# Kernel tuning notes

Measured on AMD Instinct MI355X. Metric: run time of the kernel, lower is better.

Reference implementation:

```python
import jax, jax.numpy as jnp
import numpy as np

T, B, E, H, V = 50, 64, 1024, 1024, 32000
NL = 2


def setup_inputs() -> dict:
    key = jax.random.key(0)
    ks = jax.random.split(key, 16)
    def rn(k, shape, fan_in):
        return jax.random.normal(k, shape, jnp.float32) * (1.0 / np.sqrt(fan_in))
    return {
        "word": jax.random.randint(ks[0], (B,), 0, V),
        "seq": jax.random.randint(ks[1], (T, B), 0, V),
        "emb": jax.random.normal(ks[2], (V, E), jnp.float32) * 0.05,
        "w2h_W": rn(ks[3], (H, E), E),
        "w2h_b": jnp.zeros((H,), jnp.float32),
        "W_ih0": rn(ks[4], (4 * H, 2 * E), 2 * E),
        "W_hh0": rn(ks[5], (4 * H, H), H),
        "b_ih0": jnp.zeros((4 * H,), jnp.float32),
        "b_hh0": jnp.zeros((4 * H,), jnp.float32),
        "W_ih1": rn(ks[6], (4 * H, H), H),
        "W_hh1": rn(ks[7], (4 * H, H), H),
        "b_ih1": jnp.zeros((4 * H,), jnp.float32),
        "b_hh1": jnp.zeros((4 * H,), jnp.float32),
        "dec_W": rn(ks[8], (V, H), H),
        "dec_b": jnp.zeros((V,), jnp.float32),
    }


def _lstm_layer(x, Wih, Whh, bih, bhh, h0, c0):
    """x: [T,B,D] -> hs: [T,B,H]. PyTorch gate order: i,f,g,o."""
    b = bih + bhh
    # precompute input contribution for all timesteps (one big GEMM)
    xg = jnp.einsum('tbd,gd->tbg', x, Wih) + b  # [T,B,4H]

    def step(carry, xt):
        h, c = carry
        gates = xt + h @ Whh.T
        i, f, g, o = jnp.split(gates, 4, axis=-1)
        c = jax.nn.sigmoid(f) * c + jax.nn.sigmoid(i) * jnp.tanh(g)
        h = jax.nn.sigmoid(o) * jnp.tanh(c)
        return (h, c), h

    (hT, cT), hs = jax.lax.scan(step, (h0, c0), xg)
    return hs, hT, cT


def reference(word, seq, emb, w2h_W, w2h_b, W_ih0, W_hh0, b_ih0, b_hh0,
              W_ih1, W_hh1, b_ih1, b_hh1, dec_W, dec_b):
    word_emb = emb[word]            # [B,E]
    seq_emb = emb[seq]              # [T,B,E]
    # init_hidden: c = word2hidden(word_emb) expanded over layers, h = zeros
    c0 = word_emb @ w2h_W.T + w2h_b          # [B,H]
    h0 = jnp.zeros_like(c0)
    # use_input: concat word_emb to every timestep input
    x0 = jnp.concatenate(
        [jnp.broadcast_to(word_emb[None], (T, B, E)), seq_emb], axis=-1)  # [T,B,2E]
    hs0, h0T, c0T = _lstm_layer(x0, W_ih0, W_hh0, b_ih0, b_hh0, h0, c0)
    hs1, h1T, c1T = _lstm_layer(hs0, W_ih1, W_hh1, b_ih1, b_hh1, h0, c0)
    outputs = hs1.reshape(T * B, H)
    decoded = outputs @ dec_W.T + dec_b      # [T*B, V]
    h_final = jnp.stack([h0T, h1T], 0)       # [NL,B,H]
    c_final = jnp.stack([c0T, c1T], 0)
    return decoded, h_final, c_final
```

## Files before the change

kernel.cpp:

```cpp
#include <hip/hip_runtime.h>
#include <cstddef>


static constexpr int T_ = 50, B_ = 64, E_ = 1024, H_ = 1024, V_ = 32000;
static constexpr int G_ = 4096;

typedef unsigned short u16;
typedef unsigned int u32;
typedef unsigned long long u64;
typedef __attribute__((ext_vector_type(8))) short bf16x8;
typedef __attribute__((ext_vector_type(8))) unsigned short u16x8;
typedef __attribute__((ext_vector_type(4))) float f32x4;

__device__ __forceinline__ int perm_g(int n) {
  return ((n >> 4) & 3) * H_ + (n >> 6) * 16 + (n & 15);
}
__device__ __forceinline__ u16 bf16_rn(float x) {
  union { float f; unsigned u; } a; a.f = x;
  unsigned r = a.u + 0x7fffu + ((a.u >> 16) & 1u);
  return (u16)(r >> 16);
}
__device__ __forceinline__ float bf16_f(u16 h) {
  union { float f; unsigned u; } a; a.u = ((unsigned)h) << 16;
  return a.f;
}
__device__ __forceinline__ float sigm(float x) { return 1.f / (1.f + __expf(-x)); }

__global__ void fill_zero(float* p, int n) {
  int i = blockIdx.x * blockDim.x + threadIdx.x;
  if (i < n) p[i] = 0.f;
}
__global__ void bias_perm(const float* a, const float* b, float* dst) {
  int n = blockIdx.x * 256 + threadIdx.x;
  int s = perm_g(n);
  dst[n] = a[s] + b[s];
}

__global__ void conv_w(const float* __restrict__ src, int srcld, int coloff,
                       const int* __restrict__ gidx, int PERM, int rows,
                       u16* __restrict__ dst) {
  int idx = blockIdx.x * 256 + threadIdx.x;
  int r = idx >> 7, kc = (idx & 127) << 3;
  if (r >= rows) return;
  int s = gidx ? gidx[r] : (PERM ? perm_g(r) : r);
  const float* p = src + (size_t)s * srcld + coloff + kc;
  float4 v0 = *(const float4*)p, v1 = *(const float4*)(p + 4);
  float vv[8] = {v0.x, v0.y, v0.z, v0.w, v1.x, v1.y, v1.z, v1.w};
  u16 hi[8], lo[8];
#pragma unroll
  for (int i = 0; i < 8; ++i) {
    hi[i] = bf16_rn(vv[i]);
    lo[i] = bf16_rn(vv[i] - bf16_f(hi[i]));
  }
  u16x8 c0, c1;
#pragma unroll
  for (int i = 0; i < 4; ++i) {
    c0[2 * i] = hi[i];     c0[2 * i + 1] = lo[i];
    c1[2 * i] = hi[4 + i]; c1[2 * i + 1] = lo[4 + i];
  }
  int seg = kc >> 5;
  int ch0 = (kc >> 2) & 7;
  size_t base = (size_t)r * 2048 + seg * 64;
  *(u16x8*)&dst[base + (size_t)((ch0 ^ (r & 7)) << 3)] = c0;
  *(u16x8*)&dst[base + (size_t)(((ch0 | 1) ^ (r & 7)) << 3)] = c1;
}

template<int BM, int BN, int BK, int TM, int TN>
__launch_bounds__(256)
__global__ void gemm_nt(
    const float* __restrict__ A, const int* __restrict__ Aidx, int lda,
    const float* __restrict__ W, int ldw, int koff,
    const float* __restrict__ bias, float* __restrict__ C, int ldc,
    int M, int N, int K) {
  constexpr int TX = BN / TN;
  constexpr int TY = BM / TM;
  static_assert(TX * TY == 256, "thread geometry");
  __shared__ float As[BK][BM + 4];
  __shared__ float Ws[BK][BN + 4];
  const int tid = threadIdx.x;
  const int tx = tid % TX, ty = tid / TX;
  const int m0 = blockIdx.y * BM, n0 = blockIdx.x * BN;
  float acc[TM][TN];
#pragma unroll
  for (int i = 0; i < TM; ++i)
#pragma unroll
    for (int j = 0; j < TN; ++j) acc[i][j] = 0.f;
  constexpr int AV = (BM * BK) / 4;
  constexpr int WV = (BN * BK) / 4;
  constexpr int KV = BK / 4;
  for (int k0 = 0; k0 < K; k0 += BK) {
#pragma unroll
    for (int lp = 0; lp < (AV + 255) / 256; ++lp) {
      int e = tid + lp * 256;
      if (e < AV) {
        int r = e / KV, kq = e % KV;
        int m = m0 + r;
        float4 v = make_float4(0.f, 0.f, 0.f, 0.f);
        if (m < M) {
          int row = Aidx ? Aidx[m] : m;
          v = *(const float4*)&A[(size_t)row * lda + k0 + kq * 4];
        }
        As[kq * 4 + 0][r] = v.x; As[kq * 4 + 1][r] = v.y;
        As[kq * 4 + 2][r] = v.z; As[kq * 4 + 3][r] = v.w;
      }
    }
#pragma unroll
    for (int lp = 0; lp < (WV + 255) / 256; ++lp) {
      int e = tid + lp * 256;
      if (e < WV) {
        int cc = e / KV, kq = e % KV;
        int n = n0 + cc;
        float4 v = make_float4(0.f, 0.f, 0.f, 0.f);
        if (n < N)
          v = *(const float4*)&W[(size_t)n * ldw + koff + k0 + kq * 4];
        Ws[kq * 4 + 0][cc] = v.x; Ws[kq * 4 + 1][cc] = v.y;
        Ws[kq * 4 + 2][cc] = v.z; Ws[kq * 4 + 3][cc] = v.w;
      }
    }
    __syncthreads();
#pragma unroll
    for (int kk = 0; kk < BK; ++kk) {
      float a[TM], b[TN];
#pragma unroll
      for (int i = 0; i < TM; ++i) a[i] = As[kk][ty * TM + i];
#pragma unroll
      for (int j = 0; j < TN; ++j) b[j] = Ws[kk][tx * TN + j];
#pragma unroll
      for (int i = 0; i < TM; ++i)
#pragma unroll
        for (int j = 0; j < TN; ++j)
          acc[i][j] += a[i] * b[j];
    }
    __syncthreads();
  }
#pragma unroll
  for (int i = 0; i < TM; ++i) {
    int m = m0 + ty * TM + i;
    if (m >= M) continue;
#pragma unroll
    for (int j = 0; j < TN; ++j) {
      int n = n0 + tx * TN + j;
      if (n >= N) continue;
      float v = acc[i][j];
      if (bias) v += bias[n];
      C[(size_t)m * ldc + n] = v;
    }
  }
}

__launch_bounds__(256)
__global__ void gemm_bt(const u16* __restrict__ A, int Mrows,
                        const u16* __restrict__ Wb,
                        const float* __restrict__ bias,
                        const float* __restrict__ Dadd, int ldd, int dmask,
                        float* __restrict__ C, int ldc, int N, int nbx,
                        int mt, int ord) {
  __shared__ u16 lsA[128 * 64];
  __shared__ u16 lsB[128 * 64];

  int nwg = gridDim.x, bid = blockIdx.x;
  int q = nwg >> 3, r = nwg & 7;
  int xcd = bid & 7, base = bid >> 3;
  int wg = (xcd < r ? xcd * (q + 1) : r * (q + 1) + (xcd - r) * q) + base;
  int bx, by;
  if (ord) { by = wg % mt; bx = wg / mt; } else { bx = wg % nbx; by = wg / nbx; }
  const int m0 = by * 128, n0 = bx * 128;

  const int tid = threadIdx.x, w = tid >> 6, l = tid & 63;
  const int lr = l & 15, lq = l >> 4;
  const int wm = (w >> 1) * 64, wn = (w & 1) * 64;

  f32x4 acc[4][4] = {};

  for (int kt = 0; kt < 32; ++kt) {
#pragma unroll
    for (int i = 0; i < 4; ++i) {
      int rb = w * 32 + i * 8;
      int gm = m0 + rb + (l >> 3);
      if (gm > Mrows - 1) gm = Mrows - 1;
      const u16* ga = A + (size_t)gm * 2048 + kt * 64 + (l & 7) * 8;
      __builtin_amdgcn_global_load_lds(
          (const __attribute__((address_space(1))) void*)ga,
          (__attribute__((address_space(3))) void*)(lsA + rb * 64), 16, 0, 0);
      const u16* gb = Wb + (size_t)(n0 + rb + (l >> 3)) * 2048 + kt * 64 + (l & 7) * 8;
      __builtin_amdgcn_global_load_lds(
          (const __attribute__((address_space(1))) void*)gb,
          (__attribute__((address_space(3))) void*)(lsB + rb * 64), 16, 0, 0);
    }
    asm volatile("s_waitcnt vmcnt(0)" ::: "memory");
    __syncthreads();

    bf16x8 af[4][2], bfr[4][2];
#pragma unroll
    for (int i = 0; i < 4; ++i) {
      int ar = wm + i * 16 + lr;
#pragma unroll
      for (int s = 0; s < 2; ++s)
        af[i][s] = *(const bf16x8*)&lsA[ar * 64 + (((s << 2) + lq) ^ (ar & 7)) * 8];
    }
#pragma unroll
    for (int j = 0; j < 4; ++j) {
      int br = wn + j * 16 + lr;
#pragma unroll
      for (int s = 0; s < 2; ++s)
        bfr[j][s] = *(const bf16x8*)&lsB[br * 64 + (((s << 2) + lq) ^ (br & 7)) * 8];
    }
#pragma unroll
    for (int i = 0; i < 4; ++i)
#pragma unroll
      for (int j = 0; j < 4; ++j) {
        acc[i][j] = __builtin_amdgcn_mfma_f32_16x16x32_bf16(af[i][0], bfr[j][0], acc[i][j], 0, 0, 0);
        acc[i][j] = __builtin_amdgcn_mfma_f32_16x16x32_bf16(af[i][1], bfr[j][1], acc[i][j], 0, 0, 0);
      }
    __syncthreads();
  }

#pragma unroll
  for (int i = 0; i < 4; ++i) {
    int mbase = m0 + wm + i * 16 + lq * 4;
#pragma unroll
    for (int j = 0; j < 4; ++j) {
      int n = n0 + wn + j * 16 + lr;
      float badd = bias ? bias[n] : 0.f;
#pragma unroll
      for (int rr = 0; rr < 4; ++rr) {
        int m = mbase + rr;
        if (m >= Mrows) continue;
        float v = acc[i][j][rr] + badd;
        if (Dadd) {
          int dr = (dmask < 0) ? m : (m & dmask);
          v += Dadd[(size_t)dr * ldd + n];
        }
        C[(size_t)m * ldc + n] = v;
      }
    }
  }
}

__launch_bounds__(256)
__global__ void gemm_sp(
    const float* __restrict__ A, int lda,
    const float* __restrict__ W, int ldw,
    const float* __restrict__ bias,
    float* __restrict__ C, int ldc, int M, int N, int K, int nbx) {
  __shared__ u16 As_h[128][40], As_l[128][40];
  __shared__ u16 Ws_h[128][40], Ws_l[128][40];
  int nwg = gridDim.x, bid = blockIdx.x;
  int q = nwg >> 3, r = nwg & 7;
  int xcd = bid & 7, base = bid >> 3;
  int wg = (xcd < r ? xcd * (q + 1) : r * (q + 1) + (xcd - r) * q) + base;
  int bx = wg % nbx, by = wg / nbx;
  const int m0 = by * 128, n0 = bx * 128;
  const int tid = threadIdx.x;
  const int wave = tid >> 6, lane = tid & 63;
  const int lr = lane & 15, lq = lane >> 4;
  const int wm = (wave >> 1) * 64, wn = (wave & 1) * 64;
  f32x4 acc[4][4] = {};
  for (int k0 = 0; k0 < K; k0 += 32) {
#pragma unroll
    for (int lp = 0; lp < 4; ++lp) {
      int s = tid + lp * 256;
      int row = s >> 3, kq = s & 7;
      float4 v = make_float4(0.f, 0.f, 0.f, 0.f);
      int gm = m0 + row;
      if (gm < M)
        v = *(const float4*)&A[(size_t)gm * lda + k0 + kq * 4];
      u16 h0 = bf16_rn(v.x), h1 = bf16_rn(v.y), h2 = bf16_rn(v.z), h3 = bf16_rn(v.w);
      u16 l0 = bf16_rn(v.x - bf16_f(h0)), l1 = bf16_rn(v.y - bf16_f(h1));
      u16 l2 = bf16_rn(v.z - bf16_f(h2)), l3 = bf16_rn(v.w - bf16_f(h3));
      *(uint2*)&As_h[row][kq * 4] =
          make_uint2((u32)h0 | ((u32)h1 << 16), (u32)h2 | ((u32)h3 << 16));
      *(uint2*)&As_l[row][kq * 4] =
          make_uint2((u32)l0 | ((u32)l1 << 16), (u32)l2 | ((u32)l3 << 16));
    }
#pragma unroll
    for (int lp = 0; lp < 4; ++lp) {
      int s = tid + lp * 256;
      int col = s >> 3, kq = s & 7;
      int n = n0 + col;
      float4 v = make_float4(0.f, 0.f, 0.f, 0.f);
      if (n < N)
        v = *(const float4*)&W[(size_t)n * ldw + k0 + kq * 4];
      u16 h0 = bf16_rn(v.x), h1 = bf16_rn(v.y), h2 = bf16_rn(v.z), h3 = bf16_rn(v.w);
      u16 l0 = bf16_rn(v.x - bf16_f(h0)), l1 = bf16_rn(v.y - bf16_f(h1));
      u16 l2 = bf16_rn(v.z - bf16_f(h2)), l3 = bf16_rn(v.w - bf16_f(h3));
      *(uint2*)&Ws_h[col][kq * 4] =
          make_uint2((u32)h0 | ((u32)h1 << 16), (u32)h2 | ((u32)h3 << 16));
      *(uint2*)&Ws_l[col][kq * 4] =
          make_uint2((u32)l0 | ((u32)l1 << 16), (u32)l2 | ((u32)l3 << 16));
    }
    __syncthreads();
    bf16x8 ah[4], al[4], bh[4], bl[4];
#pragma unroll
    for (int i = 0; i < 4; ++i) {
      ah[i] = *(const bf16x8*)&As_h[wm + i * 16 + lr][lq * 8];
      al[i] = *(const bf16x8*)&As_l[wm + i * 16 + lr][lq * 8];
    }
#pragma unroll
    for (int j = 0; j < 4; ++j) {
      bh[j] = *(const bf16x8*)&Ws_h[wn + j * 16 + lr][lq * 8];
      bl[j] = *(const bf16x8*)&Ws_l[wn + j * 16 + lr][lq * 8];
    }
#pragma unroll
    for (int i = 0; i < 4; ++i)
#pragma unroll
      for (int j = 0; j < 4; ++j) {
        acc[i][j] = __builtin_amdgcn_mfma_f32_16x16x32_bf16(ah[i], bh[j], acc[i][j], 0, 0, 0);
        acc[i][j] = __builtin_amdgcn_mfma_f32_16x16x32_bf16(ah[i], bl[j], acc[i][j], 0, 0, 0);
        acc[i][j] = __builtin_amdgcn_mfma_f32_16x16x32_bf16(al[i], bh[j], acc[i][j], 0, 0, 0);
      }
    __syncthreads();
  }
#pragma unroll
  for (int i = 0; i < 4; ++i) {
    int mbase = m0 + wm + i * 16 + lq * 4;
#pragma unroll
    for (int j = 0; j < 4; ++j) {
      int n = n0 + wn + j * 16 + lr;
      if (n >= N) continue;
      float badd = bias ? bias[n] : 0.f;
#pragma unroll
      for (int rr = 0; rr < 4; ++rr) {
        int m = mbase + rr;
        if (m >= M) continue;
        C[(size_t)m * ldc + n] = acc[i][j][rr] + badd;
      }
    }
  }
}

template<bool EMIT>
__launch_bounds__(512, 1)
__global__ void rnn_reg2(const u16* __restrict__ Wb, const float* __restrict__ xgall,
                         float* __restrict__ cL, float* __restrict__ hL,
                         u32* __restrict__ hs, float* __restrict__ hsf,
                         u32* __restrict__ flags, int T) {
  __shared__ float partial[8][32][68];

  const int bid = blockIdx.x;
  const int x = bid & 7, ii = bid >> 3;
  const int ct = x * 8 + (ii & 7);
  const int rg = ii >> 3;
  const int tid = threadIdx.x, w = tid >> 6, l = tid & 63;
  const int lr = l & 15, lq = l >> 4;

  const u16* WbB = Wb + (size_t)(ct * 64) * 2048;
  bf16x8 bfrag[8][4];
#pragma unroll
  for (int s = 0; s < 8; ++s)
#pragma unroll
    for (int nt = 0; nt < 4; ++nt) {
      int row = nt * 16 + lr;
      int seg = w * 4 + (s >> 1);
      int cis = ((((s & 1) << 2) + lq) ^ (lr & 7));
      bfrag[s][nt] = *(const bf16x8*)&WbB[(size_t)row * 2048 + seg * 64 + cis * 8];
    }

  const int cm = tid >> 4, cu = tid & 15;
  const int m_c = rg * 32 + cm;
  const int unit = ct * 16 + cu;
  float creg = cL[m_c * H_ + unit];

  for (int t = 0; t < T; ++t) {
    const float* xg = xgall + (size_t)t * ((size_t)B_ * G_);
    float xgv[4];
#pragma unroll
    for (int g = 0; g < 4; ++g)
      xgv[g] = xg[(size_t)m_c * G_ + ct * 64 + g * 16 + cu];

    if (t) {
      if (w == 0) {
        const u32 tgt = (u32)t;
        int guard = 0;
        for (;;) {
          u32 v = __hip_atomic_load(flags + (size_t)((rg << 6) + l) * 32,
                                    __ATOMIC_RELAXED, __HIP_MEMORY_SCOPE_AGENT);
          if (__all(v >= tgt)) break;
          if (++guard > (1 << 24)) break;
          __builtin_amdgcn_s_sleep(2);
        }
      }
    }
    __syncthreads();

    const u32* hp = hs + (size_t)t * (B_ * 1024);

    f32x4 acc[2][4] = {};
    {
      bf16x8 af[4][2];
#pragma unroll
      for (int s = 0; s < 4; ++s)
#pragma unroll
        for (int mt = 0; mt < 2; ++mt) {
          int m = rg * 32 + mt * 16 + lr;
          int seg = w * 4 + (s >> 1);
          int cis = ((((s & 1) << 2) + lq) ^ (lr & 7));
          const u64* pq = (const u64*)(hp + (size_t)m * 1024 + seg * 32 + cis * 4);
          u64 q0 = __hip_atomic_load(pq, __ATOMIC_RELAXED, __HIP_MEMORY_SCOPE_AGENT);
          u64 q1 = __hip_atomic_load(pq + 1, __ATOMIC_RELAXED, __HIP_MEMORY_SCOPE_AGENT);
          union { u64 q[2]; bf16x8 v; } cvt;
          cvt.q[0] = q0; cvt.q[1] = q1;
          af[s][mt] = cvt.v;
        }
#pragma unroll
      for (int s = 0; s < 4; ++s)
#pragma unroll
        for (int mt = 0; mt < 2; ++mt)
#pragma unroll
          for (int nt = 0; nt < 4; ++nt)
            acc[mt][nt] = __builtin_amdgcn_mfma_f32_16x16x32_bf16(
                af[s][mt], bfrag[s][nt], acc[mt][nt], 0, 0, 0);
    }
    {
      bf16x8 af[4][2];
#pragma unroll
      for (int s = 0; s < 4; ++s)
#pragma unroll
        for (int mt = 0; mt < 2; ++mt) {
          int m = rg * 32 + mt * 16 + lr;
          int seg = w * 4 + ((s + 4) >> 1);
          int cis = ((((s & 1) << 2) + lq) ^ (lr & 7));
          const u64* pq = (const u64*)(hp + (size_t)m * 1024 + seg * 32 + cis * 4);
          u64 q0 = __hip_atomic_load(pq, __ATOMIC_RELAXED, __HIP_MEMORY_SCOPE_AGENT);
          u64 q1 = __hip_atomic_load(pq + 1, __ATOMIC_RELAXED, __HIP_MEMORY_SCOPE_AGENT);
          union { u64 q[2]; bf16x8 v; } cvt;
          cvt.q[0] = q0; cvt.q[1] = q1;
          af[s][mt] = cvt.v;
        }
#pragma unroll
      for (int s = 0; s < 4; ++s)
#pragma unroll
        for (int mt = 0; mt < 2; ++mt)
#pragma unroll
          for (int nt = 0; nt < 4; ++nt)
            acc[mt][nt] = __builtin_amdgcn_mfma_f32_16x16x32_bf16(
                af[s][mt], bfrag[s + 4][nt], acc[mt][nt], 0, 0, 0);
    }

#pragma unroll
    for (int mt = 0; mt < 2; ++mt)
#pragma unroll
      for (int nt = 0; nt < 4; ++nt)
#pragma unroll
        for (int rr = 0; rr < 4; ++rr)
          partial[w][mt * 16 + lq * 4 + rr][nt * 16 + lr] = acc[mt][nt][rr];
    __syncthreads();

    float g4[4];
#pragma unroll
    for (int g = 0; g < 4; ++g) {
      float ssum = xgv[g];
#pragma unroll
      for (int p = 0; p < 8; ++p) ssum += partial[p][cm][g * 16 + cu];
      g4[g] = ssum;
    }
    float cn = sigm(g4[1]) * creg + sigm(g4[0]) * tanhf(g4[2]);
    float hn = sigm(g4[3]) * tanhf(cn);
    creg = cn;
    if (EMIT) hsf[(size_t)t * (B_ * H_) + m_c * H_ + unit] = hn;
    if (t == T - 1) { cL[m_c * H_ + unit] = cn; hL[m_c * H_ + unit] = hn; }
    u16 hh = bf16_rn(hn);
    u16 hl2 = bf16_rn(hn - bf16_f(hh));
    u32 packed = (u32)hh | ((u32)hl2 << 16);
    u32* hnext = hs + (size_t)(t + 1) * (B_ * 1024);
    u32 hidx = m_c * 1024 + ((unit >> 5) << 5) +
               ((((unit >> 2) & 7) ^ (m_c & 7)) << 2) + (unit & 3);
    __hip_atomic_store(hnext + hidx, packed, __ATOMIC_RELAXED, __HIP_MEMORY_SCOPE_AGENT);

    if (t < T - 1) {
      asm volatile("s_waitcnt vmcnt(0)" ::: "memory");
      __syncthreads();
      if (tid == 0)
        __hip_atomic_store(flags + (size_t)((rg << 6) + ct) * 32, (u32)(t + 1),
                           __ATOMIC_RELAXED, __HIP_MEMORY_SCOPE_AGENT);
    }
  }
}

__launch_bounds__(256)
__global__ void rnn_step(const u16* __restrict__ hprev, const u16* __restrict__ Wb,
                         const float* __restrict__ xg,
                         float* __restrict__ c, float* __restrict__ hf,
                         u32* __restrict__ hout) {
  __shared__ char smem[32768];
  u16* lsA = (u16*)smem;
  u16* lsB = (u16*)(smem + 16384);
  const int nt = blockIdx.x, n0 = nt * 64;
  const int tid = threadIdx.x, w = tid >> 6, l = tid & 63;
  const int lr = l & 15, lq = l >> 4;
  f32x4 acc[4] = {};
  for (int kt = 0; kt < 16; ++kt) {
#pragma unroll
    for (int i = 0; i < 4; ++i) {
      int rb = w * 16 + i * 4;
      const u16* ga = hprev + (size_t)(rb + (l >> 4)) * 2048 + kt * 128 + (l & 15) * 8;
      __builtin_amdgcn_global_load_lds(
          (const __attribute__((address_space(1))) void*)ga,
          (__attribute__((address_space(3))) void*)(lsA + rb * 128), 16, 0, 0);
      const u16* gb = Wb + (size_t)(n0 + rb + (l >> 4)) * 2048 + kt * 128 + (l & 15) * 8;
      __builtin_amdgcn_global_load_lds(
          (const __attribute__((address_space(1))) void*)gb,
          (__attribute__((address_space(3))) void*)(lsB + rb * 128), 16, 0, 0);
    }
    asm volatile("s_waitcnt vmcnt(0)" ::: "memory");
    __syncthreads();
    bf16x8 af[4];
    int ar = w * 16 + lr;
#pragma unroll
    for (int s = 0; s < 4; ++s)
      af[s] = *(const bf16x8*)&lsA[ar * 128 + (s >> 1) * 64 + ((((s & 1) << 2) + lq) ^ (ar & 7)) * 8];
#pragma unroll
    for (int j = 0; j < 4; ++j) {
      int br = j * 16 + lr;
#pragma unroll
      for (int s = 0; s < 4; ++s) {
        bf16x8 bv = *(const bf16x8*)&lsB[br * 128 + (s >> 1) * 64 + ((((s & 1) << 2) + lq) ^ (br & 7)) * 8];
        acc[j] = __builtin_amdgcn_mfma_f32_16x16x32_bf16(af[s], bv, acc[j], 0, 0, 0);
      }
    }
    __syncthreads();
  }
  float* gsh = (float*)smem;
#pragma unroll
  for (int j = 0; j < 4; ++j)
#pragma unroll
    for (int rr = 0; rr < 4; ++rr)
      gsh[(w * 16 + lq * 4 + rr) * 68 + j * 16 + lr] = acc[j][rr];
  __syncthreads();
  const int ui = tid & 15, mq = tid >> 4;
#pragma unroll
  for (int mr = 0; mr < 4; ++mr) {
    int m = mr * 16 + mq;
    float gi = gsh[m * 68 + 0 + ui]  + xg[(size_t)m * G_ + n0 + 0 + ui];
    float gf = gsh[m * 68 + 16 + ui] + xg[(size_t)m * G_ + n0 + 16 + ui];
    float gg = gsh[m * 68 + 32 + ui] + xg[(size_t)m * G_ + n0 + 32 + ui];
    float go = gsh[m * 68 + 48 + ui] + xg[(size_t)m * G_ + n0 + 48 + ui];
    int unit = nt * 16 + ui;
    int ci = m * H_ + unit;
    float cn = sigm(gf) * c[ci] + sigm(gi) * tanhf(gg);
    float hn = sigm(go) * tanhf(cn);
    c[ci] = cn;
    hf[ci] = hn;
    u16 hh = bf16_rn(hn);
    u16 hl = bf16_rn(hn - bf16_f(hh));
    u32 hidx = m * 1024 + ((unit >> 5) << 5) +
               ((((unit >> 2) & 7) ^ (m & 7)) << 2) + (unit & 3);
    hout[hidx] = (u32)hh | ((u32)hl << 16);
  }
}

extern "C" void kernel_launch(void* const* d_in, const int* in_sizes, int n_in,
                              void* d_out, int out_size, void* d_ws, size_t ws_size,
                              hipStream_t stream) {
  const int*   word  = (const int*)  d_in[0];
  const int*   seq   = (const int*)  d_in[1];
  const float* emb   = (const float*)d_in[2];
  const float* w2h_W = (const float*)d_in[3];
  const float* w2h_b = (const float*)d_in[4];
  const float* W_ih0 = (const float*)d_in[5];
  const float* W_hh0 = (const float*)d_in[6];
  const float* b_ih0 = (const float*)d_in[7];
  const float* b_hh0 = (const float*)d_in[8];
  const float* W_ih1 = (const float*)d_in[9];
  const float* W_hh1 = (const float*)d_in[10];
  const float* b_ih1 = (const float*)d_in[11];
  const float* b_hh1 = (const float*)d_in[12];
  const float* dec_W = (const float*)d_in[13];
  const float* dec_b = (const float*)d_in[14];

  float* out = (float*)d_out;
  float* hL0 = out + 102400000;
  float* hL1 = hL0 + B_ * H_;
  float* cL0 = out + 102531072;
  float* cL1 = cL0 + B_ * H_;

  float* xg0      = out;
  u16*   x0w_bf   = (u16*)(out + 13200000);
  u16*   x0seq_bf = (u16*)(out + 13300000);
  u32*   hs0slots = (u32*)(out + 16600000);
  u16*   wih0a_bf = (u16*)(out + 20000000);
  u16*   wih0b_bf = (u16*)(out + 24200000);
  u16*   wih1_bf  = (u16*)(out + 28400000);
  u16*   whh0_bf  = (u16*)(out + 32600000);
  u16*   whh1_bf  = (u16*)(out + 36800000);
  float* y_w      = out + 73800000;
  float* bias0p   = out + 74400000;
  float* bias1p   = out + 74410000;
  float* xg1      = out + 87560192;
  u32*   flg0     = (u32*)(out + 101000000);
  u32*   flg1     = (u32*)(out + 101004096);
  u32*   hbfA     = (u32*)(out + 101100000);
  u32*   hbfB     = (u32*)(out + 101200000);

  const size_t need_hs1  = (size_t)T_ * B_ * H_ * 4;
  const size_t need_full = (size_t)V_ * 2048 * 2 + (size_t)(T_ + 1) * B_ * 1024 * 4;
  const bool tier1 = ws_size >= need_full;
  const bool tier2 = !tier1 && ws_size >= need_hs1;

  u16*   decW_bf  = (u16*)d_ws;
  u32*   hs1slots = (u32*)d_ws + (size_t)V_ * 1024;
  float* hs1f     = (float*)d_ws;

  fill_zero<<<32, 256, 0, stream>>>(out + 101000000, 8192);
  fill_zero<<<256, 256, 0, stream>>>((float*)hs0slots, 65536);
  if (tier1) fill_zero<<<256, 256, 0, stream>>>((float*)hs1slots, 65536);
  bias_perm<<<16, 256, 0, stream>>>(b_ih0, b_hh0, bias0p);
  bias_perm<<<16, 256, 0, stream>>>(b_ih1, b_hh1, bias1p);

  gemm_nt<64, 64, 16, 4, 4><<<dim3(16, 1), 256, 0, stream>>>(
      emb, word, E_, w2h_W, E_, 0, w2h_b, cL0, H_, B_, H_, E_);
  gemm_nt<64, 64, 16, 4, 4><<<dim3(16, 1), 256, 0, stream>>>(
      emb, word, E_, w2h_W, E_, 0, w2h_b, cL1, H_, B_, H_, E_);

  conv_w<<<2048, 256, 0, stream>>>(W_ih0, 2 * E_, 0,  nullptr, 1, G_, wih0a_bf);
  conv_w<<<2048, 256, 0, stream>>>(W_ih0, 2 * E_, E_, nullptr, 1, G_, wih0b_bf);
  conv_w<<<2048, 256, 0, stream>>>(W_ih1, H_, 0, nullptr, 1, G_, wih1_bf);
  conv_w<<<2048, 256, 0, stream>>>(W_hh0, H_, 0, nullptr, 1, G_, whh0_bf);
  conv_w<<<2048, 256, 0, stream>>>(W_hh1, H_, 0, nullptr, 1, G_, whh1_bf);
  conv_w<<<32,   256, 0, stream>>>(emb, E_, 0, word, 0, B_, x0w_bf);
  conv_w<<<1600, 256, 0, stream>>>(emb, E_, 0, seq, 0, T_ * B_, x0seq_bf);
  if (tier1)
    conv_w<<<16000, 256, 0, stream>>>(dec_W, H_, 0, nullptr, 0, V_, decW_bf);

  gemm_bt<<<32, 256, 0, stream>>>(x0w_bf, B_, wih0a_bf, bias0p,
                                  nullptr, 0, -1, y_w, G_, G_, 32, 1, 0);
  gemm_bt<<<800, 256, 0, stream>>>(x0seq_bf, T_ * B_, wih0b_bf, nullptr,
                                   y_w, G_, 63, xg0, G_, G_, 32, 25, 0);

  rnn_reg2<false><<<128, 512, 0, stream>>>(
      whh0_bf, xg0, cL0, hL0, hs0slots, nullptr, flg0, T_);

  gemm_bt<<<800, 256, 0, stream>>>((const u16*)(hs0slots + (size_t)B_ * 1024),
                                   T_ * B_, wih1_bf, bias1p,
                                   nullptr, 0, -1, xg1, G_, G_, 32, 25, 0);

  if (tier1) {
    rnn_reg2<false><<<128, 512, 0, stream>>>(
        whh1_bf, xg1, cL1, hL1, hs1slots, nullptr, flg1, T_);
    gemm_bt<<<6250, 256, 0, stream>>>((const u16*)(hs1slots + (size_t)B_ * 1024),
                                      T_ * B_, decW_bf, dec_b,
                                      nullptr, 0, -1, out, V_, V_, 250, 25, 1);
  } else if (tier2) {
    rnn_reg2<true><<<128, 512, 0, stream>>>(
        whh1_bf, xg1, cL1, hL1, hs0slots, hs1f, flg1, T_);
    gemm_sp<<<6250, 256, 0, stream>>>(
        hs1f, H_, dec_W, H_, dec_b, out, V_, T_ * B_, V_, H_, 250);
  } else {
    for (int t = 0; t < T_; ++t) {
      const u16* hp = t ? (const u16*)((t & 1) ? hbfA : hbfB) : (const u16*)hs0slots;
      u32* ho = (t & 1) ? hbfB : hbfA;
      rnn_step<<<64, 256, 0, stream>>>(
          hp, whh1_bf, xg1 + (size_t)t * B_ * G_, cL1, hL1, ho);
      gemm_sp<<<250, 256, 0, stream>>>(
          hL1, H_, dec_W, H_, dec_b, out + (size_t)t * B_ * V_, V_, B_, V_, H_, 250);
    }
  }
}
```

Before: 1.837 ms.

## Fuse both LSTM layers into one persistent wavefront-pipelined recurrent kernel

Runs layer 0 and layer 1 recurrences concurrently in one persistent launch of 256 blocks: layer-1 blocks wait on layer-0 flags for step t+1 and compute the input projection W_ih1·h0 inline with register-resident weights, instead of waiting for layer 0 to finish and running a separate xg1 GEMM. This overlaps the two sequential recurrences and removes the intermediate GEMM and its xg1 traffic. The costs are doubled register pressure for layer-1 blocks holding two weight fragment sets, twice the MFMA work per step for those blocks, and reliance on all 256 blocks being co-resident for the spin-wait to avoid deadlock.

```diff
diff --git a/kernel.cpp b/kernel.cpp
--- a/kernel.cpp
+++ b/kernel.cpp
@@ -329,23 +329,60 @@
   }
 }
 
-template<bool EMIT>
+__device__ __forceinline__ void gemm_half(
+    const u32* __restrict__ hp, int rg, int w, int lr, int lq,
+    const bf16x8 (&bfr)[8][4], f32x4 (&acc)[2][4]) {
+#pragma unroll
+  for (int half = 0; half < 2; ++half) {
+    bf16x8 af[4][2];
+#pragma unroll
+    for (int s = 0; s < 4; ++s)
+#pragma unroll
+      for (int mt = 0; mt < 2; ++mt) {
+        int m = rg * 32 + mt * 16 + lr;
+        int seg = w * 4 + ((s + half * 4) >> 1);
+        int cis = ((((s & 1) << 2) + lq) ^ (lr & 7));
+        const u64* pq = (const u64*)(hp + (size_t)m * 1024 + seg * 32 + cis * 4);
+        u64 q0 = __hip_atomic_load(pq, __ATOMIC_RELAXED, __HIP_MEMORY_SCOPE_AGENT);
+        u64 q1 = __hip_atomic_load(pq + 1, __ATOMIC_RELAXED, __HIP_MEMORY_SCOPE_AGENT);
+        union { u64 q[2]; bf16x8 v; } cvt;
+        cvt.q[0] = q0; cvt.q[1] = q1;
+        af[s][mt] = cvt.v;
+      }
+#pragma unroll
+    for (int s = 0; s < 4; ++s)
+#pragma unroll
+      for (int mt = 0; mt < 2; ++mt)
+#pragma unroll
+        for (int nt = 0; nt < 4; ++nt)
+          acc[mt][nt] = __builtin_amdgcn_mfma_f32_16x16x32_bf16(
+              af[s][mt], bfr[s + half * 4][nt], acc[mt][nt], 0, 0, 0);
+  }
+}
+
+template<bool DUAL, bool EMIT>
 __launch_bounds__(512, 1)
-__global__ void rnn_reg2(const u16* __restrict__ Wb, const float* __restrict__ xgall,
-                         float* __restrict__ cL, float* __restrict__ hL,
-                         u32* __restrict__ hs, float* __restrict__ hsf,
-                         u32* __restrict__ flags, int T) {
+__global__ void rnn_dual(const u16* __restrict__ Whh0b, const u16* __restrict__ Whh1b,
+                         const u16* __restrict__ Wih1b,
+                         const float* __restrict__ xg0all, const float* __restrict__ bias1p,
+                         float* __restrict__ cL0, float* __restrict__ hL0,
+                         float* __restrict__ cL1, float* __restrict__ hL1,
+                         u32* __restrict__ h0s, u32* __restrict__ h1s,
+                         float* __restrict__ hsf,
+                         u32* __restrict__ flg0, u32* __restrict__ flg1, int T) {
   __shared__ float partial[8][32][68];
 
   const int bid = blockIdx.x;
-  const int x = bid & 7, ii = bid >> 3;
-  const int ct = x * 8 + (ii & 7);
-  const int rg = ii >> 3;
+  const int x = bid & 7, j = bid >> 3;
+  const int layer = DUAL ? (j & 1) : 0;
+  const int idx = DUAL ? (j >> 1) : j;
+  const int ct = x * 8 + (idx & 7);
+  const int rg = idx >> 3;
   const int tid = threadIdx.x, w = tid >> 6, l = tid & 63;
   const int lr = l & 15, lq = l >> 4;
 
-  const u16* WbB = Wb + (size_t)(ct * 64) * 2048;
-  bf16x8 bfrag[8][4];
+  const u16* WbA = (layer ? Whh1b : Whh0b) + (size_t)(ct * 64) * 2048;
+  bf16x8 bfragA[8][4];
 #pragma unroll
   for (int s = 0; s < 8; ++s)
 #pragma unroll
@@ -353,88 +390,91 @@
       int row = nt * 16 + lr;
       int seg = w * 4 + (s >> 1);
       int cis = ((((s & 1) << 2) + lq) ^ (lr & 7));
-      bfrag[s][nt] = *(const bf16x8*)&WbB[(size_t)row * 2048 + seg * 64 + cis * 8];
-    }
+      bfragA[s][nt] = *(const bf16x8*)&WbA[(size_t)row * 2048 + seg * 64 + cis * 8];
+    }
+  bf16x8 bfragX[8][4];
+  if (DUAL && layer) {
+    const u16* WbX = Wih1b + (size_t)(ct * 64) * 2048;
+#pragma unroll
+    for (int s = 0; s < 8; ++s)
+#pragma unroll
+      for (int nt = 0; nt < 4; ++nt) {
+        int row = nt * 16 + lr;
+        int seg = w * 4 + (s >> 1);
+        int cis = ((((s & 1) << 2) + lq) ^ (lr & 7));
+        bfragX[s][nt] = *(const bf16x8*)&WbX[(size_t)row * 2048 + seg * 64 + cis * 8];
+      }
+  }
 
   const int cm = tid >> 4, cu = tid & 15;
   const int m_c = rg * 32 + cm;
   const int unit = ct * 16 + cu;
+  float* cL = layer ? cL1 : cL0;
+  float* hL = layer ? hL1 : hL0;
+  u32* hsl = layer ? h1s : h0s;
+  u32* flgS = layer ? flg1 : flg0;
   float creg = cL[m_c * H_ + unit];
+  float bset[4];
+  if (layer) {
+#pragma unroll
+    for (int g = 0; g < 4; ++g)
+      bset[g] = bias1p[ct * 64 + g * 16 + cu];
+  }
 
   for (int t = 0; t < T; ++t) {
-    const float* xg = xgall + (size_t)t * ((size_t)B_ * G_);
     float xgv[4];
-#pragma unroll
-    for (int g = 0; g < 4; ++g)
-      xgv[g] = xg[(size_t)m_c * G_ + ct * 64 + g * 16 + cu];
-
-    if (t) {
-      if (w == 0) {
+    if (!layer) {
+      const float* xg = xg0all + (size_t)t * ((size_t)B_ * G_);
+#pragma unroll
+      for (int g = 0; g < 4; ++g)
+        xgv[g] = xg[(size_t)m_c * G_ + ct * 64 + g * 16 + cu];
+    } else {
+#pragma unroll
+      for (int g = 0; g < 4; ++g) xgv[g] = bset[g];
+    }
+
+    if (w == 0) {
+      if (layer) {
+        const u32 tgt0 = (u32)(t + 1);
+        int guard = 0;
+        for (;;) {
+          u32 v = __hip_atomic_load(flg0 + (size_t)((rg << 6) + l) * 32,
+                                    __ATOMIC_RELAXED, __HIP_MEMORY_SCOPE_AGENT);
+          if (__all(v >= tgt0)) break;
+          if (++guard > (1 << 23)) break;
+          __builtin_amdgcn_s_sleep(2);
+        }
+        if (t) {
+          const u32 tgt1 = (u32)t;
+          guard = 0;
+          for (;;) {
+            u32 v = __hip_atomic_load(flg1 + (size_t)((rg << 6) + l) * 32,
+                                      __ATOMIC_RELAXED, __HIP_MEMORY_SCOPE_AGENT);
+            if (__all(v >= tgt1)) break;
+            if (++guard > (1 << 23)) break;
+            __builtin_amdgcn_s_sleep(2);
+          }
+        }
+      } else if (t) {
         const u32 tgt = (u32)t;
         int guard = 0;
         for (;;) {
-          u32 v = __hip_atomic_load(flags + (size_t)((rg << 6) + l) * 32,
+          u32 v = __hip_atomic_load(flg0 + (size_t)((rg << 6) + l) * 32,
                                     __ATOMIC_RELAXED, __HIP_MEMORY_SCOPE_AGENT);
           if (__all(v >= tgt)) break;
-          if (++guard > (1 << 24)) break;
+          if (++guard > (1 << 23)) break;
           __builtin_amdgcn_s_sleep(2);
         }
       }
     }
     __syncthreads();
 
-    const u32* hp = hs + (size_t)t * (B_ * 1024);
-
     f32x4 acc[2][4] = {};
-    {
-      bf16x8 af[4][2];
-#pragma unroll
-      for (int s = 0; s < 4; ++s)
-#pragma unroll
-        for (int mt = 0; mt < 2; ++mt) {
-          int m = rg * 32 + mt * 16 + lr;
-          int seg = w * 4 + (s >> 1);
-          int cis = ((((s & 1) << 2) + lq) ^ (lr & 7));
-          const u64* pq = (const u64*)(hp + (size_t)m * 1024 + seg * 32 + cis * 4);
-          u64 q0 = __hip_atomic_load(pq, __ATOMIC_RELAXED, __HIP_MEMORY_SCOPE_AGENT);
-          u64 q1 = __hip_atomic_load(pq + 1, __ATOMIC_RELAXED, __HIP_MEMORY_SCOPE_AGENT);
-          union { u64 q[2]; bf16x8 v; } cvt;
-          cvt.q[0] = q0; cvt.q[1] = q1;
-          af[s][mt] = cvt.v;
-        }
-#pragma unroll
-      for (int s = 0; s < 4; ++s)
-#pragma unroll
-        for (int mt = 0; mt < 2; ++mt)
-#pragma unroll
-          for (int nt = 0; nt < 4; ++nt)
-            acc[mt][nt] = __builtin_amdgcn_mfma_f32_16x16x32_bf16(
-                af[s][mt], bfrag[s][nt], acc[mt][nt], 0, 0, 0);
-    }
-    {
-      bf16x8 af[4][2];
-#pragma unroll
-      for (int s = 0; s < 4; ++s)
-#pragma unroll
-        for (int mt = 0; mt < 2; ++mt) {
-          int m = rg * 32 + mt * 16 + lr;
-          int seg = w * 4 + ((s + 4) >> 1);
-          int cis = ((((s & 1) << 2) + lq) ^ (lr & 7));
-          const u64* pq = (const u64*)(hp + (size_t)m * 1024 + seg * 32 + cis * 4);
-          u64 q0 = __hip_atomic_load(pq, __ATOMIC_RELAXED, __HIP_MEMORY_SCOPE_AGENT);
-          u64 q1 = __hip_atomic_load(pq + 1, __ATOMIC_RELAXED, __HIP_MEMORY_SCOPE_AGENT);
-          union { u64 q[2]; bf16x8 v; } cvt;
-          cvt.q[0] = q0; cvt.q[1] = q1;
-          af[s][mt] = cvt.v;
-        }
-#pragma unroll
-      for (int s = 0; s < 4; ++s)
-#pragma unroll
-        for (int mt = 0; mt < 2; ++mt)
-#pragma unroll
-          for (int nt = 0; nt < 4; ++nt)
-            acc[mt][nt] = __builtin_amdgcn_mfma_f32_16x16x32_bf16(
-                af[s][mt], bfrag[s + 4][nt], acc[mt][nt], 0, 0, 0);
+    if (layer) {
+      gemm_half(h1s + (size_t)t * (B_ * 1024), rg, w, lr, lq, bfragA, acc);
+      gemm_half(h0s + (size_t)(t + 1) * (B_ * 1024), rg, w, lr, lq, bfragX, acc);
+    } else {
+      gemm_half(h0s + (size_t)t * (B_ * 1024), rg, w, lr, lq, bfragA, acc);
     }
 
 #pragma unroll
@@ -457,21 +497,21 @@
     float cn = sigm(g4[1]) * creg + sigm(g4[0]) * tanhf(g4[2]);
     float hn = sigm(g4[3]) * tanhf(cn);
     creg = cn;
-    if (EMIT) hsf[(size_t)t * (B_ * H_) + m_c * H_ + unit] = hn;
+    if (EMIT && layer) hsf[(size_t)t * (B_ * H_) + m_c * H_ + unit] = hn;
     if (t == T - 1) { cL[m_c * H_ + unit] = cn; hL[m_c * H_ + unit] = hn; }
     u16 hh = bf16_rn(hn);
     u16 hl2 = bf16_rn(hn - bf16_f(hh));
     u32 packed = (u32)hh | ((u32)hl2 << 16);
-    u32* hnext = hs + (size_t)(t + 1) * (B_ * 1024);
+    u32* hnext = hsl + (size_t)(t + 1) * (B_ * 1024);
     u32 hidx = m_c * 1024 + ((unit >> 5) << 5) +
                ((((unit >> 2) & 7) ^ (m_c & 7)) << 2) + (unit & 3);
     __hip_atomic_store(hnext + hidx, packed, __ATOMIC_RELAXED, __HIP_MEMORY_SCOPE_AGENT);
 
-    if (t < T - 1) {
+    if (!layer || t < T - 1) {
       asm volatile("s_waitcnt vmcnt(0)" ::: "memory");
       __syncthreads();
       if (tid == 0)
-        __hip_atomic_store(flags + (size_t)((rg << 6) + ct) * 32, (u32)(t + 1),
+        __hip_atomic_store(flgS + (size_t)((rg << 6) + ct) * 32, (u32)(t + 1),
                            __ATOMIC_RELAXED, __HIP_MEMORY_SCOPE_AGENT);
     }
   }
@@ -587,6 +627,7 @@
   float* bias0p   = out + 74400000;
   float* bias1p   = out + 74410000;
   float* xg1      = out + 87560192;
+  u32*   h1alt    = (u32*)(out + 91000000);
   u32*   flg0     = (u32*)(out + 101000000);
   u32*   flg1     = (u32*)(out + 101004096);
   u32*   hbfA     = (u32*)(out + 101100000);
@@ -604,6 +645,7 @@
   fill_zero<<<32, 256, 0, stream>>>(out + 101000000, 8192);
   fill_zero<<<256, 256, 0, stream>>>((float*)hs0slots, 65536);
   if (tier1) fill_zero<<<256, 256, 0, stream>>>((float*)hs1slots, 65536);
+  else if (tier2) fill_zero<<<256, 256, 0, stream>>>((float*)h1alt, 65536);
   bias_perm<<<16, 256, 0, stream>>>(b_ih0, b_hh0, bias0p);
   bias_perm<<<16, 256, 0, stream>>>(b_ih1, b_hh1, bias1p);
 
@@ -627,25 +669,26 @@
   gemm_bt<<<800, 256, 0, stream>>>(x0seq_bf, T_ * B_, wih0b_bf, nullptr,
                                    y_w, G_, 63, xg0, G_, G_, 32, 25, 0);
 
-  rnn_reg2<false><<<128, 512, 0, stream>>>(
-      whh0_bf, xg0, cL0, hL0, hs0slots, nullptr, flg0, T_);
-
-  gemm_bt<<<800, 256, 0, stream>>>((const u16*)(hs0slots + (size_t)B_ * 1024),
-                                   T_ * B_, wih1_bf, bias1p,
-                                   nullptr, 0, -1, xg1, G_, G_, 32, 25, 0);
-
   if (tier1) {
-    rnn_reg2<false><<<128, 512, 0, stream>>>(
-        whh1_bf, xg1, cL1, hL1, hs1slots, nullptr, flg1, T_);
+    rnn_dual<true, false><<<256, 512, 0, stream>>>(
+        whh0_bf, whh1_bf, wih1_bf, xg0, bias1p,
+        cL0, hL0, cL1, hL1, hs0slots, hs1slots, nullptr, flg0, flg1, T_);
     gemm_bt<<<6250, 256, 0, stream>>>((const u16*)(hs1slots + (size_t)B_ * 1024),
                                       T_ * B_, decW_bf, dec_b,
                                       nullptr, 0, -1, out, V_, V_, 250, 25, 1);
   } else if (tier2) {
-    rnn_reg2<true><<<128, 512, 0, stream>>>(
-        whh1_bf, xg1, cL1, hL1, hs0slots, hs1f, flg1, T_);
+    rnn_dual<true, true><<<256, 512, 0, stream>>>(
+        whh0_bf, whh1_bf, wih1_bf, xg0, bias1p,
+        cL0, hL0, cL1, hL1, hs0slots, h1alt, hs1f, flg0, flg1, T_);
     gemm_sp<<<6250, 256, 0, stream>>>(
         hs1f, H_, dec_W, H_, dec_b, out, V_, T_ * B_, V_, H_, 250);
   } else {
+    rnn_dual<false, false><<<128, 512, 0, stream>>>(
+        whh0_bf, whh1_bf, wih1_bf, xg0, bias1p,
+        cL0, hL0, cL1, hL1, hs0slots, nullptr, nullptr, flg0, flg1, T_);
+    gemm_bt<<<800, 256, 0, stream>>>((const u16*)(hs0slots + (size_t)B_ * 1024),
+                                     T_ * B_, wih1_bf, bias1p,
+                                     nullptr, 0, -1, xg1, G_, G_, 32, 25, 0);
     for (int t = 0; t < T_; ++t) {
       const u16* hp = t ? (const u16*)((t & 1) ? hbfA : hbfB) : (const u16*)hs0slots;
       u32* ho = (t & 1) ? hbfB : hbfA;
```

Result: slower. 1.910 ms (+4.0%).
